# Optimization experiments

Measured on AMD Instinct MI355X. Metric: run time of the kernel, lower is better.

The kernel has to match this reference:

```python
import jax, jax.numpy as jnp
import numpy as np

HUMAN_CONF = 0.7
KP_CONF = 0.5
NMS_THR = 0.5


def _cxcywh_to_xyxy(b):
    cx, cy, w, h = b[..., 0], b[..., 1], b[..., 2], b[..., 3]
    return jnp.stack([cx - 0.5 * w, cy - 0.5 * h, cx + 0.5 * w, cy + 0.5 * h], axis=-1)


def _iou_matrix(boxes):  # [Q,4] xyxy -> [Q,Q]
    area = jnp.maximum(boxes[:, 2] - boxes[:, 0], 0) * jnp.maximum(boxes[:, 3] - boxes[:, 1], 0)
    lt = jnp.maximum(boxes[:, None, :2], boxes[None, :, :2])
    rb = jnp.minimum(boxes[:, None, 2:], boxes[None, :, 2:])
    wh = jnp.maximum(rb - lt, 0)
    inter = wh[..., 0] * wh[..., 1]
    union = area[:, None] + area[None, :] - inter
    return inter / jnp.maximum(union, 1e-9)


def _nms(boxes, scores, valid, thr):
    # Greedy NMS over score-sorted boxes; invalid boxes never kept.
    Q = scores.shape[0]
    order = jnp.argsort(jnp.where(valid, scores, -jnp.inf))[::-1]
    b, v = boxes[order], valid[order]
    iou = _iou_matrix(b)
    idxs = jnp.arange(Q)

    def body(sup, i):
        keep_i = v[i] & jnp.logical_not(sup[i])
        sup = sup | (keep_i & (iou[i] > thr) & (idxs != i))
        return sup, keep_i

    _, keeps = jax.lax.scan(body, jnp.zeros(Q, bool), idxs)
    return jnp.zeros(Q, bool).at[order].set(keeps)


def _roi_kps(hm, box, sx, sy):
    # hm: [K,H,W] float, box: [4] int32 (xyxy in image coords).
    # Masked full-map argmax == ROI-crop argmax of the original (outside = -inf).
    K, H, W = hm.shape
    x1 = jnp.maximum((box[0].astype(jnp.float32) * sx).astype(jnp.int32), 0)
    y1 = jnp.maximum((box[1].astype(jnp.float32) * sy).astype(jnp.int32), 0)
    x2 = jnp.minimum((box[2].astype(jnp.float32) * sx).astype(jnp.int32) + 1, W)
    y2 = jnp.minimum((box[3].astype(jnp.float32) * sy).astype(jnp.int32) + 1, H)
    xs, ys = jnp.arange(W), jnp.arange(H)
    mask = ((ys >= y1) & (ys < y2))[:, None] & ((xs >= x1) & (xs < x2))[None, :]
    flat = jnp.where(mask[None], hm, -jnp.inf).reshape(K, -1)
    max_vals = flat.max(-1)
    idx = flat.argmax(-1)
    col = (idx % W).astype(jnp.float32)
    row = (idx // W).astype(jnp.float32)
    kps = jnp.stack([col / sx, row / sy, max_vals], -1)  # [K,3]
    ok = (x2 > x1) & (y2 > y1)
    return jnp.where(ok, kps, 0.0)


def setup_inputs() -> dict:
    key = jax.random.key(0)
    k1, k2, k3 = jax.random.split(key, 3)
    B, Q, K, Hh, Wh = 4, 100, 17, 128, 128
    return {
        "human_logits": jax.random.normal(k1, (B, Q, 2), jnp.float32) * 2.0,
        "pred_boxes": jax.random.uniform(k2, (B, Q, 4), jnp.float32),
        "pred_heatmaps": jax.random.normal(k3, (B, K, Hh, Wh), jnp.float32),
        "img_h": 512,
        "img_w": 512,
    }


def reference(human_logits, pred_boxes, pred_heatmaps, img_h, img_w):
    K, Hh, Wh = pred_heatmaps.shape[1:]
    prob = jax.nn.softmax(human_logits, -1)
    scores = prob.max(-1)          # [B,Q]
    labels = prob.argmax(-1)       # [B,Q]
    scale = jnp.array([img_w, img_h, img_w, img_h], jnp.float32)
    boxes = _cxcywh_to_xyxy(pred_boxes) * scale  # [B,Q,4] image coords
    valid = (labels == 0) & (scores >= HUMAN_CONF)
    keep = jax.vmap(lambda b, s, v: _nms(b, s, v, NMS_THR))(boxes, scores, valid)  # [B,Q] bool
    boxes_int = boxes.astype(jnp.int32)
    sx, sy = Wh / img_w, Hh / img_h
    kps = jax.vmap(lambda hm, bx: jax.vmap(lambda b: _roi_kps(hm, b, sx, sy))(bx))(
        pred_heatmaps, boxes_int)  # [B,Q,K,3]
    conf = kps[..., 2]
    kps = kps.at[..., 2].set(jnp.where(conf < KP_CONF, 0.0, conf))
    keep_f = keep.astype(jnp.float32)
    scores_out = scores * keep_f
    kps_out = kps * keep_f[:, :, None, None]
    boxes_out = boxes_int * keep[:, :, None]
    return scores_out, boxes_out, kps_out, keep
```

## Files before the change

kernel.cpp:

```cpp
#include <hip/hip_runtime.h>
#include <cmath>
#include <cfloat>

constexpr int NB = 4;
constexpr int NQ = 100;
constexpr int NK = 17;
constexpr int NH = 128;
constexpr int NW = 128;

constexpr float HUMAN_CONF = 0.7f;
constexpr float KP_CONF    = 0.5f;
constexpr float NMS_THR    = 0.5f;

constexpr int OFF_BOXES = NB * NQ;
constexpr int OFF_KPS   = NB * NQ * 5;
constexpr int OFF_KEEP  = NB * NQ * 5 + NB * NQ * NK * 3;

constexpr int NBLK = 1024;
constexpr int WAVES_PER_BATCH = (NBLK / NB) * 2;

__global__ __launch_bounds__(128) void fused_kernel(
    const float* __restrict__ logits,
    const float* __restrict__ pboxes,
    const float* __restrict__ hm,
    const int* __restrict__ img_h_p,
    const int* __restrict__ img_w_p,
    float* __restrict__ out)
{
    const int blk = blockIdx.x;
    const int t   = threadIdx.x;
    const int b   = blk & 3;
    const int sub = blk >> 2;

    __shared__ float  skey[NQ];
    __shared__ float4 srtb[104];
    __shared__ unsigned long long smask0[NQ], smask1[NQ];
    __shared__ unsigned long long svb[2];
    __shared__ unsigned long long skmask[2];
    __shared__ int sqpack[NQ];

    float4 wv4 = make_float4(0.f, 0.f, 0.f, 0.f);
    const int  line = blk * 128 + t;
    const bool doW  = line < (NB * NK * NH * NW) / 16;
    if (doW) wv4 = ((const float4*)hm)[line * 4];

    const float iw = (float)img_w_p[0];
    const float ih = (float)img_h_p[0];
    const float sxl = (float)NW / iw;
    const float syl = (float)NH / ih;

    if (t < 104) srtb[t] = make_float4(0.f, 0.f, 0.f, 0.f);

    float score = 0.f, x1 = 0.f, y1 = 0.f, x2 = 0.f, y2 = 0.f;
    bool valid = false;
    if (t < NQ) {
        const float2 lg = ((const float2*)logits)[b * NQ + t];
        const float m  = fmaxf(lg.x, lg.y);
        const float e0 = expf(lg.x - m);
        const float e1 = expf(lg.y - m);
        score = fmaxf(e0, e1) / (e0 + e1);
        const bool lab0 = (lg.x >= lg.y);

        const float4 pb = ((const float4*)pboxes)[b * NQ + t];
        x1 = (pb.x - 0.5f * pb.z) * iw;
        y1 = (pb.y - 0.5f * pb.w) * ih;
        x2 = (pb.x + 0.5f * pb.z) * iw;
        y2 = (pb.y + 0.5f * pb.w) * ih;

        valid = lab0 && (score >= HUMAN_CONF);
        skey[t] = valid ? score : -INFINITY;
    }
    {
        const unsigned long long vb = __ballot(valid);
        if ((t & 63) == 0) svb[t >> 6] = vb;
    }
    __syncthreads();

    const int V = __popcll(svb[0]) + __popcll(svb[1]);

    int r = 0;
    if (t < NQ) {
        const float key = valid ? score : -INFINITY;
        for (int j = 0; j < NQ; j += 4) {
            const float a0 = skey[j + 0];
            const float a1 = skey[j + 1];
            const float a2 = skey[j + 2];
            const float a3 = skey[j + 3];
            r += (a0 > key || (a0 == key && (j + 0) > t)) ? 1 : 0;
            r += (a1 > key || (a1 == key && (j + 1) > t)) ? 1 : 0;
            r += (a2 > key || (a2 == key && (j + 2) > t)) ? 1 : 0;
            r += (a3 > key || (a3 == key && (j + 3) > t)) ? 1 : 0;
        }
        if (valid) srtb[r] = make_float4(x1, y1, x2, y2);
    }
    __syncthreads();

    if (valid) {
        unsigned long long m0 = 0ull, m1 = 0ull;
        const float aa = fmaxf(x2 - x1, 0.f) * fmaxf(y2 - y1, 0.f);
        const int Vp = (V + 3) & ~3;
        for (int j = 0; j < Vp; j += 4) {
            #pragma unroll
            for (int u = 0; u < 4; ++u) {
                const float4 bb = srtb[j + u];
                const float ba = fmaxf(bb.z - bb.x, 0.f) * fmaxf(bb.w - bb.y, 0.f);
                const float lx = fmaxf(x1, bb.x);
                const float ly = fmaxf(y1, bb.y);
                const float rx = fminf(x2, bb.z);
                const float ry = fminf(y2, bb.w);
                const float wv = fmaxf(rx - lx, 0.f);
                const float hv = fmaxf(ry - ly, 0.f);
                const float inter = wv * hv;
                const float uni = aa + ba - inter;
                const float iou = inter / fmaxf(uni, 1e-9f);
                if (iou > NMS_THR) {
                    const int jj = j + u;
                    if (jj < 64) m0 |= 1ull << jj; else m1 |= 1ull << (jj - 64);
                }
            }
        }
        smask0[r] = m0; smask1[r] = m1;
    }
    __syncthreads();

    if (t < 64) {
        const unsigned long long rm0 = smask0[t];
        const unsigned long long rm1 = smask1[t];

        unsigned long long rem0 = (V >= 64) ? ~0ull : ((1ull << V) - 1ull);
        unsigned long long rem1 = 0ull;
        if (V > 64) { const int v1 = V - 64; rem1 = (v1 >= 64) ? ~0ull : ((1ull << v1) - 1ull); }

        unsigned long long k0 = 0ull, k1 = 0ull;
        while (rem0 | rem1) {
            int i;
            unsigned long long bit0 = 0ull, bit1 = 0ull;
            if (rem0) { i = __builtin_ctzll(rem0); bit0 = 1ull << i; }
            else      { const int j = __builtin_ctzll(rem1); i = 64 + j; bit1 = 1ull << j; }
            k0 |= bit0; k1 |= bit1;
            unsigned long long row0, row1;
            if (i < 64) {
                row0 = __shfl(rm0, i);
                row1 = __shfl(rm1, i);
            } else {
                row0 = smask0[i];
                row1 = smask1[i];
            }
            rem0 &= ~(row0 | bit0);
            rem1 &= ~(row1 | bit1);
        }
        if (t == 0) { skmask[0] = k0; skmask[1] = k1; }
    }
    __syncthreads();

    if (t < NQ) {
        const unsigned long long k0s = skmask[0];
        const unsigned long long k1s = skmask[1];
        int kp = 0;
        if (valid) kp = (r < 64) ? (int)((k0s >> r) & 1ull)
                                 : (int)((k1s >> (r - 64)) & 1ull);

        const int bi0 = (int)x1;
        const int bi1 = (int)y1;
        const int bi2 = (int)x2;
        const int bi3 = (int)y2;

        const int x1i = max((int)((float)bi0 * sxl), 0);
        const int y1i = max((int)((float)bi1 * syl), 0);
        const int x2i = min((int)((float)bi2 * sxl) + 1, NW);
        const int y2i = min((int)((float)bi3 * syl) + 1, NH);
        const bool live = kp && (x2i > x1i) && (y2i > y1i);

        sqpack[t] = live ? (x1i | (y1i << 8) | (x2i << 16) | (y2i << 24)) : 0;

        if (sub == 0) {
            const int gi = b * NQ + t;
            out[gi] = score * (float)kp;
            out[OFF_BOXES + gi * 4 + 0] = (float)(bi0 * kp);
            out[OFF_BOXES + gi * 4 + 1] = (float)(bi1 * kp);
            out[OFF_BOXES + gi * 4 + 2] = (float)(bi2 * kp);
            out[OFF_BOXES + gi * 4 + 3] = (float)(bi3 * kp);
            out[OFF_KEEP + gi] = (float)kp;
        }
    }
    __syncthreads();

    if (doW) asm volatile("" :: "v"(wv4.x), "v"(wv4.y), "v"(wv4.z), "v"(wv4.w));

    const int lane = t & 63;
    const int wvid = sub * 2 + (t >> 6);

    for (int item = wvid; item < NQ * NK; item += WAVES_PER_BATCH) {
        const int q = item / NK;
        const int k = item - q * NK;
        const int gi = b * NQ + q;
        float* kout = out + OFF_KPS + (size_t)gi * (NK * 3) + k * 3;

        const int pack = sqpack[q];
        if (pack == 0) {
            if (lane < 3) kout[lane] = 0.0f;
            continue;
        }

        const int x1r = pack & 255;
        const int y1r = (pack >> 8) & 255;
        const int x2r = (pack >> 16) & 255;
        const int y2r = (pack >> 24) & 255;

        const float4* __restrict__ b4 =
            (const float4*)(hm + (size_t)(b * NK + k) * (NH * NW));

        const int xa     = x1r & ~3;
        const int C4     = (x2r - xa + 3) >> 2;
        const int R      = y2r - y1r;
        const int total4 = R * C4;
        const unsigned M = (C4 > 1) ? (0xFFFFFFFFu / (unsigned)C4 + 1u) : 0u;

        float best = -INFINITY;
        int   bidx = 0x7fffffff;

        auto proc = [&](int idx, float4 v) {
            const int row = (C4 == 1) ? idx : (int)__umulhi((unsigned)idx, M);
            const int xb  = xa + (idx - row * C4) * 4;
            const int g   = (y1r + row) * NW + xb;
            const float v0 = (xb + 0 >= x1r && xb + 0 < x2r) ? v.x : -INFINITY;
            const float v1 = (xb + 1 >= x1r && xb + 1 < x2r) ? v.y : -INFINITY;
            const float v2 = (xb + 2 >= x1r && xb + 2 < x2r) ? v.z : -INFINITY;
            const float v3 = (xb + 3 < x2r) ? v.w : -INFINITY;
            if (v0 > best) { best = v0; bidx = g + 0; }
            if (v1 > best) { best = v1; bidx = g + 1; }
            if (v2 > best) { best = v2; bidx = g + 2; }
            if (v3 > best) { best = v3; bidx = g + 3; }
        };
        auto caddr = [&](int idx) {
            const int row = (C4 == 1) ? idx : (int)__umulhi((unsigned)idx, M);
            return (y1r + row) * (NW / 4) + (xa >> 2) + (idx - row * C4);
        };

        int idx = lane;
        for (; idx + 192 < total4; idx += 256) {
            const int a0 = caddr(idx), a1 = caddr(idx + 64), a2 = caddr(idx + 128), a3 = caddr(idx + 192);
            const float4 v0 = b4[a0];
            const float4 v1 = b4[a1];
            const float4 v2 = b4[a2];
            const float4 v3 = b4[a3];
            proc(idx, v0);
            proc(idx + 64, v1);
            proc(idx + 128, v2);
            proc(idx + 192, v3);
        }
        for (; idx < total4; idx += 64) proc(idx, b4[caddr(idx)]);

        for (int off = 32; off >= 1; off >>= 1) {
            const float ov = __shfl_down(best, off);
            const int   oi = __shfl_down(bidx, off);
            if (ov > best || (ov == best && oi < bidx)) { best = ov; bidx = oi; }
        }

        if (lane == 0) {
            const int col = bidx & (NW - 1);
            const int row = bidx >> 7;
            float conf = best;
            if (conf < KP_CONF) conf = 0.0f;
            kout[0] = (float)col / sxl;
            kout[1] = (float)row / syl;
            kout[2] = conf;
        }
    }
}

extern "C" void kernel_launch(void* const* d_in, const int* in_sizes, int n_in,
                              void* d_out, int out_size, void* d_ws, size_t ws_size,
                              hipStream_t stream) {
    const float* logits = (const float*)d_in[0];
    const float* pboxes = (const float*)d_in[1];
    const float* hm     = (const float*)d_in[2];
    const int*   img_h  = (const int*)d_in[3];
    const int*   img_w  = (const int*)d_in[4];
    float* out = (float*)d_out;

    fused_kernel<<<NBLK, 128, 0, stream>>>(logits, pboxes, hm, img_h, img_w, out);
}
```

Before: 96.83 us.

## Cost-balance keypoint ROI work across blocks via prefix-sum binning

Replaces the round-robin assignment of (query, keypoint) items to waves with a cost-weighted partition. Each item's ROI size is prefix-summed, and every block builds a shared-memory list of the items whose cost midpoint falls in its bin. Each item is then reduced by the whole 128-thread block, combining the two waves through shared memory. The aim is to even out per-block load when ROI sizes vary a lot, at the cost of an extra prefix pass, an LDS atomic list build, and a block-wide barrier per item.

```diff
diff --git a/kernel.cpp b/kernel.cpp
--- a/kernel.cpp
+++ b/kernel.cpp
@@ -17,7 +17,6 @@
 constexpr int OFF_KEEP  = NB * NQ * 5 + NB * NQ * NK * 3;
 
 constexpr int NBLK = 1024;
-constexpr int WAVES_PER_BATCH = (NBLK / NB) * 2;
 
 __global__ __launch_bounds__(128) void fused_kernel(
     const float* __restrict__ logits,
@@ -38,6 +37,12 @@
     __shared__ unsigned long long svb[2];
     __shared__ unsigned long long skmask[2];
     __shared__ int sqpack[NQ];
+    __shared__ int scq[NQ];
+    __shared__ int sSq[NQ];
+    __shared__ unsigned short slist[NQ * NK];
+    __shared__ int scount;
+    __shared__ float sredv[2][2];
+    __shared__ int   sredi[2][2];
 
     float4 wv4 = make_float4(0.f, 0.f, 0.f, 0.f);
     const int  line = blk * 128 + t;
@@ -50,6 +55,7 @@
     const float syl = (float)NH / ih;
 
     if (t < 104) srtb[t] = make_float4(0.f, 0.f, 0.f, 0.f);
+    if (t == 0) scount = 0;
 
     float score = 0.f, x1 = 0.f, y1 = 0.f, x2 = 0.f, y2 = 0.f;
     bool valid = false;
@@ -173,6 +179,14 @@
 
         sqpack[t] = live ? (x1i | (y1i << 8) | (x2i << 16) | (y2i << 24)) : 0;
 
+        int cost = 0;
+        if (live) {
+            const int xa = x1i & ~3;
+            const int C4 = (x2i - xa + 3) >> 2;
+            cost = (y2i - y1i) * C4;
+        }
+        scq[t] = cost;
+
         if (sub == 0) {
             const int gi = b * NQ + t;
             out[gi] = score * (float)kp;
@@ -187,25 +201,52 @@
 
     if (doW) asm volatile("" :: "v"(wv4.x), "v"(wv4.y), "v"(wv4.z), "v"(wv4.w));
 
-    const int lane = t & 63;
-    const int wvid = sub * 2 + (t >> 6);
-
-    for (int item = wvid; item < NQ * NK; item += WAVES_PER_BATCH) {
-        const int q = item / NK;
-        const int k = item - q * NK;
-        const int gi = b * NQ + q;
-        float* kout = out + OFF_KPS + (size_t)gi * (NK * 3) + k * 3;
-
+    int pref = 0, tcq = 0;
+    for (int j = 0; j < NQ; j += 4) {
+        #pragma unroll
+        for (int u = 0; u < 4; ++u) {
+            const int c = scq[j + u];
+            tcq += c;
+            pref += ((j + u) < t) ? c : 0;
+        }
+    }
+    if (t < NQ) sSq[t] = pref;
+    __syncthreads();
+
+    const int TC = 17 * tcq;
+    const int binsz2 = 2 * ((TC + 255) >> 8);
+
+    for (int g = t; g < NQ * NK; g += 128) {
+        const int q = g / NK;
+        const int k = g - q * NK;
         const int pack = sqpack[q];
         if (pack == 0) {
-            if (lane < 3) kout[lane] = 0.0f;
-            continue;
-        }
-
+            if ((g & 255) == sub) {
+                float* kout = out + OFF_KPS + (size_t)(b * NQ + q) * (NK * 3) + k * 3;
+                kout[0] = 0.0f; kout[1] = 0.0f; kout[2] = 0.0f;
+            }
+        } else {
+            const int c  = scq[q];
+            const int m2 = 34 * sSq[q] + (2 * k + 1) * c;
+            if (m2 / binsz2 == sub) {
+                const int pos = atomicAdd(&scount, 1);
+                slist[pos] = (unsigned short)g;
+            }
+        }
+    }
+    __syncthreads();
+
+    const int icount = scount;
+    for (int n = 0; n < icount; ++n) {
+        const int id = slist[n];
+        const int q  = id / NK;
+        const int k  = id - q * NK;
+        const int pack = sqpack[q];
         const int x1r = pack & 255;
         const int y1r = (pack >> 8) & 255;
         const int x2r = (pack >> 16) & 255;
         const int y2r = (pack >> 24) & 255;
+        const int gi  = b * NQ + q;
 
         const float4* __restrict__ b4 =
             (const float4*)(hm + (size_t)(b * NK + k) * (NH * NW));
@@ -237,31 +278,37 @@
             return (y1r + row) * (NW / 4) + (xa >> 2) + (idx - row * C4);
         };
 
-        int idx = lane;
-        for (; idx + 192 < total4; idx += 256) {
-            const int a0 = caddr(idx), a1 = caddr(idx + 64), a2 = caddr(idx + 128), a3 = caddr(idx + 192);
+        int idx = t;
+        for (; idx + 384 < total4; idx += 512) {
+            const int a0 = caddr(idx), a1 = caddr(idx + 128), a2 = caddr(idx + 256), a3 = caddr(idx + 384);
             const float4 v0 = b4[a0];
             const float4 v1 = b4[a1];
             const float4 v2 = b4[a2];
             const float4 v3 = b4[a3];
             proc(idx, v0);
-            proc(idx + 64, v1);
-            proc(idx + 128, v2);
-            proc(idx + 192, v3);
-        }
-        for (; idx < total4; idx += 64) proc(idx, b4[caddr(idx)]);
+            proc(idx + 128, v1);
+            proc(idx + 256, v2);
+            proc(idx + 384, v3);
+        }
+        for (; idx < total4; idx += 128) proc(idx, b4[caddr(idx)]);
 
         for (int off = 32; off >= 1; off >>= 1) {
             const float ov = __shfl_down(best, off);
             const int   oi = __shfl_down(bidx, off);
             if (ov > best || (ov == best && oi < bidx)) { best = ov; bidx = oi; }
         }
-
-        if (lane == 0) {
-            const int col = bidx & (NW - 1);
-            const int row = bidx >> 7;
-            float conf = best;
+        if ((t & 63) == 0) { sredv[n & 1][t >> 6] = best; sredi[n & 1][t >> 6] = bidx; }
+        __syncthreads();
+
+        if (t == 0) {
+            float bv = sredv[n & 1][0]; int bi = sredi[n & 1][0];
+            const float ov = sredv[n & 1][1]; const int oi = sredi[n & 1][1];
+            if (ov > bv || (ov == bv && oi < bi)) { bv = ov; bi = oi; }
+            const int col = bi & (NW - 1);
+            const int row = bi >> 7;
+            float conf = bv;
             if (conf < KP_CONF) conf = 0.0f;
+            float* kout = out + OFF_KPS + (size_t)gi * (NK * 3) + k * 3;
             kout[0] = (float)col / sxl;
             kout[1] = (float)row / syl;
             kout[2] = conf;
```

Result: slower. 119.6 us (+23.5%).

## Balance ROI argmax work across waves by cost-weighted prefix-sum binning

Applied to the files above, without the earlier changes.

Replaces the round-robin assignment of (query, keypoint) items to waves with a cost-aware partition. Each item's cost is its ROI size in float4 plus a fixed overhead, and a prefix sum over queries maps each item's midpoint into one of 512 equal-cost bins per batch. The intent is to stop waves that drew large boxes from becoming stragglers. In exchange every wave scans all 1700 items with a ballot and does a serial prefix-sum loop, and zero-filling of dead items moves to a separate strided loop.

```diff
diff --git a/kernel.cpp b/kernel.cpp
--- a/kernel.cpp
+++ b/kernel.cpp
@@ -17,7 +17,7 @@
 constexpr int OFF_KEEP  = NB * NQ * 5 + NB * NQ * NK * 3;
 
 constexpr int NBLK = 1024;
-constexpr int WAVES_PER_BATCH = (NBLK / NB) * 2;
+constexpr int OV   = 96;
 
 __global__ __launch_bounds__(128) void fused_kernel(
     const float* __restrict__ logits,
@@ -38,6 +38,8 @@
     __shared__ unsigned long long svb[2];
     __shared__ unsigned long long skmask[2];
     __shared__ int sqpack[NQ];
+    __shared__ int scq[NQ];
+    __shared__ int sSq[NQ];
 
     float4 wv4 = make_float4(0.f, 0.f, 0.f, 0.f);
     const int  line = blk * 128 + t;
@@ -173,6 +175,14 @@
 
         sqpack[t] = live ? (x1i | (y1i << 8) | (x2i << 16) | (y2i << 24)) : 0;
 
+        int cost = 0;
+        if (live) {
+            const int xa = x1i & ~3;
+            const int C4 = (x2i - xa + 3) >> 2;
+            cost = (y2i - y1i) * C4 + OV;
+        }
+        scq[t] = cost;
+
         if (sub == 0) {
             const int gi = b * NQ + t;
             out[gi] = score * (float)kp;
@@ -187,84 +197,119 @@
 
     if (doW) asm volatile("" :: "v"(wv4.x), "v"(wv4.y), "v"(wv4.z), "v"(wv4.w));
 
+    int pref = 0, tcq = 0;
+    for (int j = 0; j < NQ; j += 4) {
+        #pragma unroll
+        for (int u = 0; u < 4; ++u) {
+            const int c = scq[j + u];
+            tcq += c;
+            pref += ((j + u) < t) ? c : 0;
+        }
+    }
+    if (t < NQ) sSq[t] = pref;
+    __syncthreads();
+
+    for (int g = t; g < NQ * NK; g += 128) {
+        const int q = g / NK;
+        if (sqpack[q] == 0 && (g & 255) == sub) {
+            const int k = g - q * NK;
+            float* kout = out + OFF_KPS + (size_t)(b * NQ + q) * (NK * 3) + k * 3;
+            kout[0] = 0.0f; kout[1] = 0.0f; kout[2] = 0.0f;
+        }
+    }
+
     const int lane = t & 63;
-    const int wvid = sub * 2 + (t >> 6);
-
-    for (int item = wvid; item < NQ * NK; item += WAVES_PER_BATCH) {
-        const int q = item / NK;
-        const int k = item - q * NK;
-        const int gi = b * NQ + q;
-        float* kout = out + OFF_KPS + (size_t)gi * (NK * 3) + k * 3;
-
-        const int pack = sqpack[q];
-        if (pack == 0) {
-            if (lane < 3) kout[lane] = 0.0f;
-            continue;
-        }
-
-        const int x1r = pack & 255;
-        const int y1r = (pack >> 8) & 255;
-        const int x2r = (pack >> 16) & 255;
-        const int y2r = (pack >> 24) & 255;
-
-        const float4* __restrict__ b4 =
-            (const float4*)(hm + (size_t)(b * NK + k) * (NH * NW));
-
-        const int xa     = x1r & ~3;
-        const int C4     = (x2r - xa + 3) >> 2;
-        const int R      = y2r - y1r;
-        const int total4 = R * C4;
-        const unsigned M = (C4 > 1) ? (0xFFFFFFFFu / (unsigned)C4 + 1u) : 0u;
-
-        float best = -INFINITY;
-        int   bidx = 0x7fffffff;
-
-        auto proc = [&](int idx, float4 v) {
-            const int row = (C4 == 1) ? idx : (int)__umulhi((unsigned)idx, M);
-            const int xb  = xa + (idx - row * C4) * 4;
-            const int g   = (y1r + row) * NW + xb;
-            const float v0 = (xb + 0 >= x1r && xb + 0 < x2r) ? v.x : -INFINITY;
-            const float v1 = (xb + 1 >= x1r && xb + 1 < x2r) ? v.y : -INFINITY;
-            const float v2 = (xb + 2 >= x1r && xb + 2 < x2r) ? v.z : -INFINITY;
-            const float v3 = (xb + 3 < x2r) ? v.w : -INFINITY;
-            if (v0 > best) { best = v0; bidx = g + 0; }
-            if (v1 > best) { best = v1; bidx = g + 1; }
-            if (v2 > best) { best = v2; bidx = g + 2; }
-            if (v3 > best) { best = v3; bidx = g + 3; }
-        };
-        auto caddr = [&](int idx) {
-            const int row = (C4 == 1) ? idx : (int)__umulhi((unsigned)idx, M);
-            return (y1r + row) * (NW / 4) + (xa >> 2) + (idx - row * C4);
-        };
-
-        int idx = lane;
-        for (; idx + 192 < total4; idx += 256) {
-            const int a0 = caddr(idx), a1 = caddr(idx + 64), a2 = caddr(idx + 128), a3 = caddr(idx + 192);
-            const float4 v0 = b4[a0];
-            const float4 v1 = b4[a1];
-            const float4 v2 = b4[a2];
-            const float4 v3 = b4[a3];
-            proc(idx, v0);
-            proc(idx + 64, v1);
-            proc(idx + 128, v2);
-            proc(idx + 192, v3);
-        }
-        for (; idx < total4; idx += 64) proc(idx, b4[caddr(idx)]);
-
-        for (int off = 32; off >= 1; off >>= 1) {
-            const float ov = __shfl_down(best, off);
-            const int   oi = __shfl_down(bidx, off);
-            if (ov > best || (ov == best && oi < bidx)) { best = ov; bidx = oi; }
-        }
-
-        if (lane == 0) {
-            const int col = bidx & (NW - 1);
-            const int row = bidx >> 7;
-            float conf = best;
-            if (conf < KP_CONF) conf = 0.0f;
-            kout[0] = (float)col / sxl;
-            kout[1] = (float)row / syl;
-            kout[2] = conf;
+    const int wbin = sub * 2 + (t >> 6);
+    const int TC2  = 17 * tcq;
+    const int binsz2 = max(2 * ((TC2 + 511) >> 9), 2);
+
+    for (int g0 = 0; g0 < NQ * NK; g0 += 64) {
+        const int g = g0 + lane;
+        bool mine = false;
+        if (g < NQ * NK) {
+            const int q = g / NK;
+            const int k = g - q * NK;
+            const int c = scq[q];
+            if (c != 0) {
+                const int m2 = 34 * sSq[q] + (2 * k + 1) * c;
+                mine = (m2 / binsz2) == wbin;
+            }
+        }
+        unsigned long long mask = __ballot(mine);
+        while (mask) {
+            const int bit = __builtin_ctzll(mask);
+            mask &= mask - 1;
+            const int id = g0 + bit;
+
+            const int q  = id / NK;
+            const int k  = id - q * NK;
+            const int pack = sqpack[q];
+            const int x1r = pack & 255;
+            const int y1r = (pack >> 8) & 255;
+            const int x2r = (pack >> 16) & 255;
+            const int y2r = (pack >> 24) & 255;
+            const int gi  = b * NQ + q;
+
+            const float4* __restrict__ b4 =
+                (const float4*)(hm + (size_t)(b * NK + k) * (NH * NW));
+
+            const int xa     = x1r & ~3;
+            const int C4     = (x2r - xa + 3) >> 2;
+            const int R      = y2r - y1r;
+            const int total4 = R * C4;
+            const unsigned M = (C4 > 1) ? (0xFFFFFFFFu / (unsigned)C4 + 1u) : 0u;
+
+            float best = -INFINITY;
+            int   bidx = 0x7fffffff;
+
+            auto proc = [&](int idx, float4 v) {
+                const int row = (C4 == 1) ? idx : (int)__umulhi((unsigned)idx, M);
+                const int xb  = xa + (idx - row * C4) * 4;
+                const int g2  = (y1r + row) * NW + xb;
+                const float v0 = (xb + 0 >= x1r && xb + 0 < x2r) ? v.x : -INFINITY;
+                const float v1 = (xb + 1 >= x1r && xb + 1 < x2r) ? v.y : -INFINITY;
+                const float v2 = (xb + 2 >= x1r && xb + 2 < x2r) ? v.z : -INFINITY;
+                const float v3 = (xb + 3 < x2r) ? v.w : -INFINITY;
+                if (v0 > best) { best = v0; bidx = g2 + 0; }
+                if (v1 > best) { best = v1; bidx = g2 + 1; }
+                if (v2 > best) { best = v2; bidx = g2 + 2; }
+                if (v3 > best) { best = v3; bidx = g2 + 3; }
+            };
+            auto caddr = [&](int idx) {
+                const int row = (C4 == 1) ? idx : (int)__umulhi((unsigned)idx, M);
+                return (y1r + row) * (NW / 4) + (xa >> 2) + (idx - row * C4);
+            };
+
+            int idx = lane;
+            for (; idx + 192 < total4; idx += 256) {
+                const int a0 = caddr(idx), a1 = caddr(idx + 64), a2 = caddr(idx + 128), a3 = caddr(idx + 192);
+                const float4 v0 = b4[a0];
+                const float4 v1 = b4[a1];
+                const float4 v2 = b4[a2];
+                const float4 v3 = b4[a3];
+                proc(idx, v0);
+                proc(idx + 64, v1);
+                proc(idx + 128, v2);
+                proc(idx + 192, v3);
+            }
+            for (; idx < total4; idx += 64) proc(idx, b4[caddr(idx)]);
+
+            for (int off = 32; off >= 1; off >>= 1) {
+                const float ov = __shfl_down(best, off);
+                const int   oi = __shfl_down(bidx, off);
+                if (ov > best || (ov == best && oi < bidx)) { best = ov; bidx = oi; }
+            }
+
+            if (lane == 0) {
+                const int col = bidx & (NW - 1);
+                const int row = bidx >> 7;
+                float conf = best;
+                if (conf < KP_CONF) conf = 0.0f;
+                float* kout = out + OFF_KPS + (size_t)gi * (NK * 3) + k * 3;
+                kout[0] = (float)col / sxl;
+                kout[1] = (float)row / syl;
+                kout[2] = conf;
+            }
         }
     }
 }
```

After: 98.10 us. No clear change (+1.3%).
